# Kernel optimization log

Hardware: AMD Instinct MI355X
Metric: run time of the kernel (lower is better)

The kernel has to match this reference:

```python
import jax, jax.numpy as jnp
import numpy as np

# dims matching init_kwargs
U, T, S, K = 2048, 200, 10, 20   # users, history_length, slate_size, num_topics
DE, DU, V, H = 32, 32, 100000, 16  # doc_embed_dim, user_embed_dim, num_docs, rnn hidden
D_IN = DE + (S + 1) + (S + 1) * K + 1  # 264 concatenated feature width
LEAKY_ALPHA = 0.3  # keras LeakyReLU default


def setup_inputs() -> dict:
    key = jax.random.key(0)
    ks = jax.random.split(key, 9)
    slate_doc_quality_history = jax.random.normal(ks[0], (U, T, S), jnp.float32)
    slate_doc_features_history = jax.random.normal(ks[1], (U, T, S, K), jnp.float32)
    docid_history = jax.random.randint(ks[2], (U, T), 0, V + 1)  # 0 is the masked id
    ctime_history = jax.random.uniform(ks[3], (U, T), jnp.float32)
    # learned parameters
    emb_table = jax.random.normal(ks[4], (V + 1, DE), jnp.float32) * 0.05
    Wx = jax.random.normal(ks[5], (D_IN, H), jnp.float32) * (1.0 / np.sqrt(D_IN))
    Wh = jax.random.normal(ks[6], (H, H), jnp.float32) * (1.0 / np.sqrt(H))
    b_rnn = jnp.zeros((H,), jnp.float32)
    Wd = jax.random.normal(ks[7], (H, DU), jnp.float32) * (1.0 / np.sqrt(H))
    b_dense = jnp.zeros((DU,), jnp.float32)
    return dict(
        slate_doc_quality_history=slate_doc_quality_history,
        slate_doc_features_history=slate_doc_features_history,
        docid_history=docid_history,
        ctime_history=ctime_history,
        emb_table=emb_table, Wx=Wx, Wh=Wh, b_rnn=b_rnn, Wd=Wd, b_dense=b_dense,
    )


def reference(slate_doc_quality_history, slate_doc_features_history, docid_history,
              ctime_history, emb_table, Wx, Wh, b_rnn, Wd, b_dense):
    B, Tlen = docid_history.shape
    # embedding lookup; mask_zero=True -> timesteps with id==0 are skipped by the RNN
    emb = emb_table[docid_history]                                   # [U,T,DE]
    mask = docid_history != 0                                        # [U,T]
    # append zero quality column -> [U,T,S+1]
    q = jnp.concatenate([slate_doc_quality_history,
                         jnp.zeros((B, Tlen, 1), slate_doc_quality_history.dtype)], axis=-1)
    # append zero feature row on slate axis, flatten -> [U,T,(S+1)*K]
    f = jnp.concatenate([slate_doc_features_history,
                         jnp.zeros((B, Tlen, 1, K), slate_doc_features_history.dtype)], axis=-2)
    f = f.reshape(B, Tlen, -1)
    x = jnp.concatenate([emb, q, f, ctime_history[..., None]], axis=-1)  # [U,T,D_IN]

    # SimpleRNN(16): h_t = tanh(x_t Wx + h_{t-1} Wh + b); masked steps keep previous h
    pre = jnp.einsum('btd,dh->bth', x, Wx) + b_rnn                   # [U,T,H]

    def step(h, inp):
        pre_t, m_t = inp                                             # [U,H], [U]
        h_new = jnp.tanh(pre_t + h @ Wh)
        h = jnp.where(m_t[:, None], h_new, h)
        return h, None

    h0 = jnp.zeros((B, Wh.shape[0]), x.dtype)
    hT, _ = jax.lax.scan(step, h0, (pre.transpose(1, 0, 2), mask.T))
    # LeakyReLU(alpha=0.3) then Dense -> user embeddings [U, DU]
    a = jnp.where(hT >= 0, hT, LEAKY_ALPHA * hT)
    return a @ Wd + b_dense
```

## Files before the change

kernel.cpp:

```cpp
#include <hip/hip_runtime.h>

#define U_   2048
#define T_   200
#define H_   16
#define DU_  32
#define KP   288

typedef __attribute__((ext_vector_type(8))) short bf16x8;
typedef __attribute__((ext_vector_type(4))) float f32x4;

__device__ __forceinline__ unsigned short bf16_rne(float x) {
    unsigned u = __float_as_uint(x);
    return (unsigned short)((u + 0x7FFFu + ((u >> 16) & 1u)) >> 16);
}

__device__ __forceinline__ void cvt8(const float* x, bf16x8& hi, bf16x8& lo) {
    union { bf16x8 v; unsigned u[4]; } H, L;
#pragma unroll
    for (int i = 0; i < 4; ++i) {
        const unsigned short h0 = bf16_rne(x[2 * i]), h1 = bf16_rne(x[2 * i + 1]);
        const float r0 = x[2 * i]     - __uint_as_float((unsigned)h0 << 16);
        const float r1 = x[2 * i + 1] - __uint_as_float((unsigned)h1 << 16);
        H.u[i] = (unsigned)h0 | ((unsigned)h1 << 16);
        L.u[i] = (unsigned)bf16_rne(r0) | ((unsigned)bf16_rne(r1) << 16);
    }
    hi = H.v; lo = L.v;
}

__global__ __launch_bounds__(256) void k_wprep(
    const float* __restrict__ Wx,
    unsigned short* __restrict__ WThi, unsigned short* __restrict__ WTlo)
{
    const int idx = blockIdx.x * 256 + threadIdx.x;
    if (idx >= 16 * KP) return;
    const int n = idx / KP, k = idx - n * KP;
    const int s = k >> 5, kk = k & 31;
    float wv = 0.f;
    if (s < 7)       { if (k < 200) wv = Wx[(43 + k) * H_ + n]; }
    else if (s == 7) { wv = Wx[kk * H_ + n]; }
    else             { if (kk < 10) wv = Wx[(32 + kk) * H_ + n];
                       else if (kk == 10) wv = Wx[263 * H_ + n]; }
    const unsigned short h = bf16_rne(wv);
    WThi[idx] = h;
    WTlo[idx] = bf16_rne(wv - __uint_as_float((unsigned)h << 16));
}

__global__ __launch_bounds__(256, 3) void k_pre(
    const float* __restrict__ qh, const float* __restrict__ f,
    const int* __restrict__ docid, const float* __restrict__ ct,
    const float* __restrict__ emb,
    const unsigned short* __restrict__ WThi,
    const unsigned short* __restrict__ WTlo,
    const float* __restrict__ brnn, float* __restrict__ pre)
{
    __shared__ float pane[4][16 * 204];
    const int t = threadIdx.x, l = t & 63, w = t >> 6;
    const int tile = blockIdx.x * 4 + w;
    const int rbase = tile * 16;
    const int r = l & 15, qd = l >> 4;
    const int pos = rbase + r;

    const char* fsrc = (const char*)f + (size_t)rbase * 800;
    float4 buf[13];
#pragma unroll
    for (int m = 0; m < 13; ++m)
        if (m < 12 || l < 32)
            buf[m] = *(const float4*)(fsrc + (size_t)(m * 64 + l) * 16);

    const int did = docid[pos];
    const float4 e0 = *(const float4*)(emb + (size_t)did * 32 + qd * 8);
    const float4 e1 = *(const float4*)(emb + (size_t)did * 32 + qd * 8 + 4);

    float qx[8];
#pragma unroll
    for (int i = 0; i < 8; ++i) qx[i] = 0.f;
    if (qd == 0) {
#pragma unroll
        for (int j = 0; j < 4; ++j) {
            float2 v = *(const float2*)(qh + (size_t)pos * 10 + 2 * j);
            qx[2 * j] = v.x; qx[2 * j + 1] = v.y;
        }
    } else if (qd == 1) {
        qx[0] = qh[(size_t)pos * 10 + 8];
        qx[1] = qh[(size_t)pos * 10 + 9];
        qx[2] = ct[pos];
    }
    const float bias = brnn[r];

    float* pn = pane[w];
#pragma unroll
    for (int m = 0; m < 13; ++m) {
        const int g = m * 64 + l;
        if (g < 800) *(float4*)(pn + 4 * (g + g / 50)) = buf[m];
    }

    f32x4 acc = {bias, bias, bias, bias};

#pragma unroll
    for (int s = 0; s < 7; ++s) {
        float xr[8];
        if (s < 6 || qd == 0) {
            const float4 a0 = *(const float4*)(pn + r * 204 + s * 32 + qd * 8);
            const float4 a1 = *(const float4*)(pn + r * 204 + s * 32 + qd * 8 + 4);
            xr[0] = a0.x; xr[1] = a0.y; xr[2] = a0.z; xr[3] = a0.w;
            xr[4] = a1.x; xr[5] = a1.y; xr[6] = a1.z; xr[7] = a1.w;
        } else {
#pragma unroll
            for (int i = 0; i < 8; ++i) xr[i] = 0.f;
        }
        bf16x8 ah, al; cvt8(xr, ah, al);
        const bf16x8 bh = *(const bf16x8*)(WThi + r * KP + s * 32 + qd * 8);
        const bf16x8 bl = *(const bf16x8*)(WTlo + r * KP + s * 32 + qd * 8);
        acc = __builtin_amdgcn_mfma_f32_16x16x32_bf16(ah, bh, acc, 0, 0, 0);
        acc = __builtin_amdgcn_mfma_f32_16x16x32_bf16(al, bh, acc, 0, 0, 0);
        acc = __builtin_amdgcn_mfma_f32_16x16x32_bf16(ah, bl, acc, 0, 0, 0);
    }

    {
        float xr[8] = {e0.x, e0.y, e0.z, e0.w, e1.x, e1.y, e1.z, e1.w};
        bf16x8 ah, al; cvt8(xr, ah, al);
        const bf16x8 bh = *(const bf16x8*)(WThi + r * KP + 7 * 32 + qd * 8);
        const bf16x8 bl = *(const bf16x8*)(WTlo + r * KP + 7 * 32 + qd * 8);
        acc = __builtin_amdgcn_mfma_f32_16x16x32_bf16(ah, bh, acc, 0, 0, 0);
        acc = __builtin_amdgcn_mfma_f32_16x16x32_bf16(al, bh, acc, 0, 0, 0);
        acc = __builtin_amdgcn_mfma_f32_16x16x32_bf16(ah, bl, acc, 0, 0, 0);
    }
    {
        bf16x8 ah, al; cvt8(qx, ah, al);
        const bf16x8 bh = *(const bf16x8*)(WThi + r * KP + 8 * 32 + qd * 8);
        const bf16x8 bl = *(const bf16x8*)(WTlo + r * KP + 8 * 32 + qd * 8);
        acc = __builtin_amdgcn_mfma_f32_16x16x32_bf16(ah, bh, acc, 0, 0, 0);
        acc = __builtin_amdgcn_mfma_f32_16x16x32_bf16(al, bh, acc, 0, 0, 0);
        acc = __builtin_amdgcn_mfma_f32_16x16x32_bf16(ah, bl, acc, 0, 0, 0);
    }

#pragma unroll
    for (int i = 0; i < 4; ++i)
        pre[(size_t)(rbase + qd * 4 + i) * H_ + r] = acc[i];
}

__device__ __forceinline__ float tanh_fast(float x) {
    float e = __expf(2.f * x);
    return 1.f - 2.f / (e + 1.f);
}

__global__ __launch_bounds__(64) void k_rnn(
    const float* __restrict__ pre, const int* __restrict__ docid,
    const float* __restrict__ Wh, const float* __restrict__ Wd,
    const float* __restrict__ bd, float* __restrict__ out)
{
    const int tid = threadIdx.x;
    const int l = tid & 15;
    const int u = (blockIdx.x * 64 + tid) >> 4;

    const float* prow = pre + (size_t)u * T_ * H_;
    const int* drow = docid + (size_t)u * T_;

    float wh[16];
#pragma unroll
    for (int k = 0; k < 16; ++k) wh[k] = Wh[((l ^ k) << 4) | l];

    float h = 0.f;

    float pb0 = prow[0 * H_ + l], pb1 = prow[1 * H_ + l],
          pb2 = prow[2 * H_ + l], pb3 = prow[3 * H_ + l];
    int   m0 = drow[0], m1 = drow[1], m2 = drow[2], m3 = drow[3];

    for (int tb = 0; tb < T_; tb += 4) {
#pragma unroll
        for (int s = 0; s < 4; ++s) {
            float p; int m;
            if      (s == 0) { p = pb0; m = m0; }
            else if (s == 1) { p = pb1; m = m1; }
            else if (s == 2) { p = pb2; m = m2; }
            else             { p = pb3; m = m3; }

            int tn = tb + 4 + s; if (tn > T_ - 1) tn = T_ - 1;
            float pn = prow[tn * H_ + l];
            int   mn = drow[tn];
            if      (s == 0) { pb0 = pn; m0 = mn; }
            else if (s == 1) { pb1 = pn; m1 = mn; }
            else if (s == 2) { pb2 = pn; m2 = mn; }
            else             { pb3 = pn; m3 = mn; }

            float a0 = p, a1 = 0.f, a2 = 0.f, a3 = 0.f;
#pragma unroll
            for (int k = 0; k < 16; k += 4) {
                a0 += __shfl_xor(h, k + 0, 16) * wh[k + 0];
                a1 += __shfl_xor(h, k + 1, 16) * wh[k + 1];
                a2 += __shfl_xor(h, k + 2, 16) * wh[k + 2];
                a3 += __shfl_xor(h, k + 3, 16) * wh[k + 3];
            }
            float accv = (a0 + a1) + (a2 + a3);
            float th = tanh_fast(accv);
            h = (m != 0) ? th : h;
        }
    }

    float a = (h >= 0.f) ? h : 0.3f * h;

    float wd0[16], wd1[16];
#pragma unroll
    for (int k = 0; k < 16; ++k) {
        int j = l ^ k;
        wd0[k] = Wd[j * DU_ + l];
        wd1[k] = Wd[j * DU_ + l + 16];
    }
    float o0 = bd[l], o1 = bd[l + 16];
#pragma unroll
    for (int k = 0; k < 16; ++k) {
        float av = __shfl_xor(a, k, 16);
        o0 += av * wd0[k];
        o1 += av * wd1[k];
    }
    out[(size_t)u * DU_ + l] = o0;
    out[(size_t)u * DU_ + l + 16] = o1;
}

extern "C" void kernel_launch(void* const* d_in, const int* in_sizes, int n_in,
                              void* d_out, int out_size, void* d_ws, size_t ws_size,
                              hipStream_t stream) {
    const float* qh    = (const float*)d_in[0];
    const float* f     = (const float*)d_in[1];
    const int*   docid = (const int*)  d_in[2];
    const float* ct    = (const float*)d_in[3];
    const float* emb   = (const float*)d_in[4];
    const float* Wx    = (const float*)d_in[5];
    const float* Wh    = (const float*)d_in[6];
    const float* brnn  = (const float*)d_in[7];
    const float* Wd    = (const float*)d_in[8];
    const float* bd    = (const float*)d_in[9];
    float* out = (float*)d_out;

    float* pre = (float*)d_ws;
    unsigned short* WThi = (unsigned short*)((char*)d_ws + (size_t)U_ * T_ * H_ * 4);
    unsigned short* WTlo = WThi + 16 * KP;

    k_wprep<<<(16 * KP + 255) / 256, 256, 0, stream>>>(Wx, WThi, WTlo);
    k_pre<<<(U_ * T_) / 64, 256, 0, stream>>>(qh, f, docid, ct, emb, WThi, WTlo, brnn, pre);
    k_rnn<<<(U_ * H_) / 64, 64, 0, stream>>>(pre, docid, Wh, Wd, bd, out);
}
```

Before: 153.2 us.

## Make k_pre waves loop over multiple tiles with register prefetch of next tile

Each wave in the input-projection kernel now processes 8 consecutive 16-row tiles instead of one. Inside the loop it issues the global loads for the next tile's features, quality, ctime and embedding rows before running the MFMA work on the current tile, so load latency overlaps compute. The grid shrinks by the same factor of 8. The trade-off is fewer resident waves to hide memory latency, plus more live registers for the double-buffered data.

```diff
diff --git a/kernel.cpp b/kernel.cpp
--- a/kernel.cpp
+++ b/kernel.cpp
@@ -5,6 +5,7 @@
 #define H_   16
 #define DU_  32
 #define KP   288
+#define NT   8
 
 typedef __attribute__((ext_vector_type(8))) short bf16x8;
 typedef __attribute__((ext_vector_type(4))) float f32x4;
@@ -55,88 +56,118 @@
 {
     __shared__ float pane[4][16 * 204];
     const int t = threadIdx.x, l = t & 63, w = t >> 6;
-    const int tile = blockIdx.x * 4 + w;
-    const int rbase = tile * 16;
+    const int wid = blockIdx.x * 4 + w;
+    const int tbase = wid * NT;
     const int r = l & 15, qd = l >> 4;
-    const int pos = rbase + r;
-
-    const char* fsrc = (const char*)f + (size_t)rbase * 800;
+
+    float* pn = pane[w];
+    const char* fB = (const char*)f;
+    const float bias = brnn[r];
+
     float4 buf[13];
-#pragma unroll
-    for (int m = 0; m < 13; ++m)
-        if (m < 12 || l < 32)
-            buf[m] = *(const float4*)(fsrc + (size_t)(m * 64 + l) * 16);
-
-    const int did = docid[pos];
-    const float4 e0 = *(const float4*)(emb + (size_t)did * 32 + qd * 8);
-    const float4 e1 = *(const float4*)(emb + (size_t)did * 32 + qd * 8 + 4);
-
+    float4 e0, e1;
     float qx[8];
-#pragma unroll
-    for (int i = 0; i < 8; ++i) qx[i] = 0.f;
-    if (qd == 0) {
-#pragma unroll
-        for (int j = 0; j < 4; ++j) {
-            float2 v = *(const float2*)(qh + (size_t)pos * 10 + 2 * j);
-            qx[2 * j] = v.x; qx[2 * j + 1] = v.y;
-        }
-    } else if (qd == 1) {
-        qx[0] = qh[(size_t)pos * 10 + 8];
-        qx[1] = qh[(size_t)pos * 10 + 9];
-        qx[2] = ct[pos];
-    }
-    const float bias = brnn[r];
-
-    float* pn = pane[w];
-#pragma unroll
-    for (int m = 0; m < 13; ++m) {
-        const int g = m * 64 + l;
-        if (g < 800) *(float4*)(pn + 4 * (g + g / 50)) = buf[m];
-    }
-
-    f32x4 acc = {bias, bias, bias, bias};
-
-#pragma unroll
-    for (int s = 0; s < 7; ++s) {
-        float xr[8];
-        if (s < 6 || qd == 0) {
-            const float4 a0 = *(const float4*)(pn + r * 204 + s * 32 + qd * 8);
-            const float4 a1 = *(const float4*)(pn + r * 204 + s * 32 + qd * 8 + 4);
-            xr[0] = a0.x; xr[1] = a0.y; xr[2] = a0.z; xr[3] = a0.w;
-            xr[4] = a1.x; xr[5] = a1.y; xr[6] = a1.z; xr[7] = a1.w;
-        } else {
-#pragma unroll
-            for (int i = 0; i < 8; ++i) xr[i] = 0.f;
-        }
-        bf16x8 ah, al; cvt8(xr, ah, al);
-        const bf16x8 bh = *(const bf16x8*)(WThi + r * KP + s * 32 + qd * 8);
-        const bf16x8 bl = *(const bf16x8*)(WTlo + r * KP + s * 32 + qd * 8);
-        acc = __builtin_amdgcn_mfma_f32_16x16x32_bf16(ah, bh, acc, 0, 0, 0);
-        acc = __builtin_amdgcn_mfma_f32_16x16x32_bf16(al, bh, acc, 0, 0, 0);
-        acc = __builtin_amdgcn_mfma_f32_16x16x32_bf16(ah, bl, acc, 0, 0, 0);
-    }
+    int did_nxt = 0;
+
+    auto LOADF = [&](int tile) {
+#pragma unroll
+        for (int m = 0; m < 13; ++m)
+            if (m < 12 || l < 32)
+                buf[m] = *(const float4*)(fB + (size_t)tile * 12800 + (size_t)(m * 64 + l) * 16);
+    };
+    auto LOADQ = [&](int tile, float* dst) {
+        const int pos = tile * 16 + r;
+#pragma unroll
+        for (int j = 0; j < 8; ++j) dst[j] = 0.f;
+        if (qd == 0) {
+#pragma unroll
+            for (int j = 0; j < 4; ++j) {
+                float2 v = *(const float2*)(qh + (size_t)pos * 10 + 2 * j);
+                dst[2 * j] = v.x; dst[2 * j + 1] = v.y;
+            }
+        } else if (qd == 1) {
+            dst[0] = qh[(size_t)pos * 10 + 8];
+            dst[1] = qh[(size_t)pos * 10 + 9];
+            dst[2] = ct[pos];
+        }
+    };
 
     {
-        float xr[8] = {e0.x, e0.y, e0.z, e0.w, e1.x, e1.y, e1.z, e1.w};
-        bf16x8 ah, al; cvt8(xr, ah, al);
-        const bf16x8 bh = *(const bf16x8*)(WThi + r * KP + 7 * 32 + qd * 8);
-        const bf16x8 bl = *(const bf16x8*)(WTlo + r * KP + 7 * 32 + qd * 8);
-        acc = __builtin_amdgcn_mfma_f32_16x16x32_bf16(ah, bh, acc, 0, 0, 0);
-        acc = __builtin_amdgcn_mfma_f32_16x16x32_bf16(al, bh, acc, 0, 0, 0);
-        acc = __builtin_amdgcn_mfma_f32_16x16x32_bf16(ah, bl, acc, 0, 0, 0);
-    }
-    {
-        bf16x8 ah, al; cvt8(qx, ah, al);
-        const bf16x8 bh = *(const bf16x8*)(WThi + r * KP + 8 * 32 + qd * 8);
-        const bf16x8 bl = *(const bf16x8*)(WTlo + r * KP + 8 * 32 + qd * 8);
-        acc = __builtin_amdgcn_mfma_f32_16x16x32_bf16(ah, bh, acc, 0, 0, 0);
-        acc = __builtin_amdgcn_mfma_f32_16x16x32_bf16(al, bh, acc, 0, 0, 0);
-        acc = __builtin_amdgcn_mfma_f32_16x16x32_bf16(ah, bl, acc, 0, 0, 0);
-    }
-
-#pragma unroll
-    for (int i = 0; i < 4; ++i)
-        pre[(size_t)(rbase + qd * 4 + i) * H_ + r] = acc[i];
+        const int did0 = docid[tbase * 16 + r];
+        LOADF(tbase);
+        LOADQ(tbase, qx);
+        e0 = *(const float4*)(emb + (size_t)did0 * 32 + qd * 8);
+        e1 = *(const float4*)(emb + (size_t)did0 * 32 + qd * 8 + 4);
+        if (NT > 1) did_nxt = docid[(tbase + 1) * 16 + r];
+    }
+
+#pragma unroll 1
+    for (int i = 0; i < NT; ++i) {
+        const int rbase = (tbase + i) * 16;
+
+#pragma unroll
+        for (int m = 0; m < 13; ++m) {
+            const int g = m * 64 + l;
+            if (g < 800) *(float4*)(pn + 4 * (g + g / 50)) = buf[m];
+        }
+
+        const float4 ce0 = e0, ce1 = e1;
+        float cq[8];
+#pragma unroll
+        for (int j = 0; j < 8; ++j) cq[j] = qx[j];
+
+        if (i + 1 < NT) {
+            LOADF(tbase + i + 1);
+            LOADQ(tbase + i + 1, qx);
+            const int dd = did_nxt;
+            e0 = *(const float4*)(emb + (size_t)dd * 32 + qd * 8);
+            e1 = *(const float4*)(emb + (size_t)dd * 32 + qd * 8 + 4);
+            if (i + 2 < NT) did_nxt = docid[(tbase + i + 2) * 16 + r];
+        }
+
+        f32x4 acc = {bias, bias, bias, bias};
+
+#pragma unroll
+        for (int s = 0; s < 7; ++s) {
+            float xr[8];
+            if (s < 6 || qd == 0) {
+                const float4 a0 = *(const float4*)(pn + r * 204 + s * 32 + qd * 8);
+                const float4 a1 = *(const float4*)(pn + r * 204 + s * 32 + qd * 8 + 4);
+                xr[0] = a0.x; xr[1] = a0.y; xr[2] = a0.z; xr[3] = a0.w;
+                xr[4] = a1.x; xr[5] = a1.y; xr[6] = a1.z; xr[7] = a1.w;
+            } else {
+#pragma unroll
+                for (int j = 0; j < 8; ++j) xr[j] = 0.f;
+            }
+            bf16x8 ah, al; cvt8(xr, ah, al);
+            const bf16x8 bh = *(const bf16x8*)(WThi + r * KP + s * 32 + qd * 8);
+            const bf16x8 bl = *(const bf16x8*)(WTlo + r * KP + s * 32 + qd * 8);
+            acc = __builtin_amdgcn_mfma_f32_16x16x32_bf16(ah, bh, acc, 0, 0, 0);
+            acc = __builtin_amdgcn_mfma_f32_16x16x32_bf16(al, bh, acc, 0, 0, 0);
+            acc = __builtin_amdgcn_mfma_f32_16x16x32_bf16(ah, bl, acc, 0, 0, 0);
+        }
+        {
+            float xr[8] = {ce0.x, ce0.y, ce0.z, ce0.w, ce1.x, ce1.y, ce1.z, ce1.w};
+            bf16x8 ah, al; cvt8(xr, ah, al);
+            const bf16x8 bh = *(const bf16x8*)(WThi + r * KP + 7 * 32 + qd * 8);
+            const bf16x8 bl = *(const bf16x8*)(WTlo + r * KP + 7 * 32 + qd * 8);
+            acc = __builtin_amdgcn_mfma_f32_16x16x32_bf16(ah, bh, acc, 0, 0, 0);
+            acc = __builtin_amdgcn_mfma_f32_16x16x32_bf16(al, bh, acc, 0, 0, 0);
+            acc = __builtin_amdgcn_mfma_f32_16x16x32_bf16(ah, bl, acc, 0, 0, 0);
+        }
+        {
+            bf16x8 ah, al; cvt8(cq, ah, al);
+            const bf16x8 bh = *(const bf16x8*)(WThi + r * KP + 8 * 32 + qd * 8);
+            const bf16x8 bl = *(const bf16x8*)(WTlo + r * KP + 8 * 32 + qd * 8);
+            acc = __builtin_amdgcn_mfma_f32_16x16x32_bf16(ah, bh, acc, 0, 0, 0);
+            acc = __builtin_amdgcn_mfma_f32_16x16x32_bf16(al, bh, acc, 0, 0, 0);
+            acc = __builtin_amdgcn_mfma_f32_16x16x32_bf16(ah, bl, acc, 0, 0, 0);
+        }
+
+#pragma unroll
+        for (int ii = 0; ii < 4; ++ii)
+            pre[(size_t)(rbase + qd * 4 + ii) * H_ + r] = acc[ii];
+    }
 }
 
 __device__ __forceinline__ float tanh_fast(float x) {
@@ -237,6 +268,6 @@
     unsigned short* WTlo = WThi + 16 * KP;
 
     k_wprep<<<(16 * KP + 255) / 256, 256, 0, stream>>>(Wx, WThi, WTlo);
-    k_pre<<<(U_ * T_) / 64, 256, 0, stream>>>(qh, f, docid, ct, emb, WThi, WTlo, brnn, pre);
+    k_pre<<<(U_ * T_) / (64 * NT), 256, 0, stream>>>(qh, f, docid, ct, emb, WThi, WTlo, brnn, pre);
     k_rnn<<<(U_ * H_) / 64, 64, 0, stream>>>(pre, docid, Wh, Wd, bd, out);
 }
```

Result: slower. 356.9 us (+133.0%).

## Double-buffer feature tiles via direct global-to-LDS loads in persistent k_pre waves

Applied to the files above, without the earlier changes.

Restructures k_pre so each single-wave block processes eight 16-row tiles in a loop. The next tile's features are prefetched straight into LDS with global_load_lds while the current tile goes through the MFMAs. An XOR swizzle on the LDS layout replaces the old padded layout to avoid bank conflicts. The aim is to hide the latency of the dominant feature stream and drop the register round-trip; the cost is fewer, smaller blocks and a full vmcnt(0) wait every iteration.

```diff
diff --git a/kernel.cpp b/kernel.cpp
--- a/kernel.cpp
+++ b/kernel.cpp
@@ -5,6 +5,7 @@
 #define H_   16
 #define DU_  32
 #define KP   288
+#define NT   8
 
 typedef __attribute__((ext_vector_type(8))) short bf16x8;
 typedef __attribute__((ext_vector_type(4))) float f32x4;
@@ -25,6 +26,12 @@
         L.u[i] = (unsigned)bf16_rne(r0) | ((unsigned)bf16_rne(r1) << 16);
     }
     hi = H.v; lo = L.v;
+}
+
+__device__ __forceinline__ void g2l16(const void* g, void* l) {
+    __builtin_amdgcn_global_load_lds(
+        (const __attribute__((address_space(1))) void*)g,
+        (__attribute__((address_space(3))) void*)l, 16, 0, 0);
 }
 
 __global__ __launch_bounds__(256) void k_wprep(
@@ -45,7 +52,7 @@
     WTlo[idx] = bf16_rne(wv - __uint_as_float((unsigned)h << 16));
 }
 
-__global__ __launch_bounds__(256, 3) void k_pre(
+__global__ __launch_bounds__(64) void k_pre(
     const float* __restrict__ qh, const float* __restrict__ f,
     const int* __restrict__ docid, const float* __restrict__ ct,
     const float* __restrict__ emb,
@@ -53,90 +60,117 @@
     const unsigned short* __restrict__ WTlo,
     const float* __restrict__ brnn, float* __restrict__ pre)
 {
-    __shared__ float pane[4][16 * 204];
-    const int t = threadIdx.x, l = t & 63, w = t >> 6;
-    const int tile = blockIdx.x * 4 + w;
-    const int rbase = tile * 16;
+    __shared__ float pane[2][13 * 64 * 4];
+    const int l = threadIdx.x;
     const int r = l & 15, qd = l >> 4;
-    const int pos = rbase + r;
-
-    const char* fsrc = (const char*)f + (size_t)rbase * 800;
-    float4 buf[13];
-#pragma unroll
-    for (int m = 0; m < 13; ++m)
-        if (m < 12 || l < 32)
-            buf[m] = *(const float4*)(fsrc + (size_t)(m * 64 + l) * 16);
-
-    const int did = docid[pos];
-    const float4 e0 = *(const float4*)(emb + (size_t)did * 32 + qd * 8);
-    const float4 e1 = *(const float4*)(emb + (size_t)did * 32 + qd * 8 + 4);
-
-    float qx[8];
-#pragma unroll
-    for (int i = 0; i < 8; ++i) qx[i] = 0.f;
-    if (qd == 0) {
-#pragma unroll
-        for (int j = 0; j < 4; ++j) {
-            float2 v = *(const float2*)(qh + (size_t)pos * 10 + 2 * j);
-            qx[2 * j] = v.x; qx[2 * j + 1] = v.y;
-        }
-    } else if (qd == 1) {
-        qx[0] = qh[(size_t)pos * 10 + 8];
-        qx[1] = qh[(size_t)pos * 10 + 9];
-        qx[2] = ct[pos];
-    }
+    const int tbase = blockIdx.x * NT;
+    const char* fB = (const char*)f;
+
+    int off[13];
+#pragma unroll
+    for (int m = 0; m < 13; ++m) {
+        const int slot = m * 64 + l;
+        if (slot < 800) {
+            const int p = slot / 50, g2 = slot - 50 * p;
+            const int gr = (g2 < 48) ? (g2 ^ (p & 7)) : g2;
+            off[m] = p * 800 + gr * 16;
+        } else off[m] = 0;
+    }
+
+    auto STAGE = [&](int tile, int b) {
+        const char* src = fB + (size_t)tile * 12800;
+        char* dst = (char*)pane[b];
+#pragma unroll
+        for (int m = 0; m < 13; ++m)
+            g2l16(src + off[m], dst + m * 1024);
+    };
+
     const float bias = brnn[r];
-
-    float* pn = pane[w];
-#pragma unroll
-    for (int m = 0; m < 13; ++m) {
-        const int g = m * 64 + l;
-        if (g < 800) *(float4*)(pn + 4 * (g + g / 50)) = buf[m];
-    }
-
-    f32x4 acc = {bias, bias, bias, bias};
-
-#pragma unroll
-    for (int s = 0; s < 7; ++s) {
-        float xr[8];
-        if (s < 6 || qd == 0) {
-            const float4 a0 = *(const float4*)(pn + r * 204 + s * 32 + qd * 8);
-            const float4 a1 = *(const float4*)(pn + r * 204 + s * 32 + qd * 8 + 4);
-            xr[0] = a0.x; xr[1] = a0.y; xr[2] = a0.z; xr[3] = a0.w;
-            xr[4] = a1.x; xr[5] = a1.y; xr[6] = a1.z; xr[7] = a1.w;
-        } else {
-#pragma unroll
-            for (int i = 0; i < 8; ++i) xr[i] = 0.f;
-        }
-        bf16x8 ah, al; cvt8(xr, ah, al);
-        const bf16x8 bh = *(const bf16x8*)(WThi + r * KP + s * 32 + qd * 8);
-        const bf16x8 bl = *(const bf16x8*)(WTlo + r * KP + s * 32 + qd * 8);
-        acc = __builtin_amdgcn_mfma_f32_16x16x32_bf16(ah, bh, acc, 0, 0, 0);
-        acc = __builtin_amdgcn_mfma_f32_16x16x32_bf16(al, bh, acc, 0, 0, 0);
-        acc = __builtin_amdgcn_mfma_f32_16x16x32_bf16(ah, bl, acc, 0, 0, 0);
-    }
-
-    {
-        float xr[8] = {e0.x, e0.y, e0.z, e0.w, e1.x, e1.y, e1.z, e1.w};
-        bf16x8 ah, al; cvt8(xr, ah, al);
-        const bf16x8 bh = *(const bf16x8*)(WThi + r * KP + 7 * 32 + qd * 8);
-        const bf16x8 bl = *(const bf16x8*)(WTlo + r * KP + 7 * 32 + qd * 8);
-        acc = __builtin_amdgcn_mfma_f32_16x16x32_bf16(ah, bh, acc, 0, 0, 0);
-        acc = __builtin_amdgcn_mfma_f32_16x16x32_bf16(al, bh, acc, 0, 0, 0);
-        acc = __builtin_amdgcn_mfma_f32_16x16x32_bf16(ah, bl, acc, 0, 0, 0);
-    }
-    {
-        bf16x8 ah, al; cvt8(qx, ah, al);
-        const bf16x8 bh = *(const bf16x8*)(WThi + r * KP + 8 * 32 + qd * 8);
-        const bf16x8 bl = *(const bf16x8*)(WTlo + r * KP + 8 * 32 + qd * 8);
-        acc = __builtin_amdgcn_mfma_f32_16x16x32_bf16(ah, bh, acc, 0, 0, 0);
-        acc = __builtin_amdgcn_mfma_f32_16x16x32_bf16(al, bh, acc, 0, 0, 0);
-        acc = __builtin_amdgcn_mfma_f32_16x16x32_bf16(ah, bl, acc, 0, 0, 0);
-    }
-
-#pragma unroll
-    for (int i = 0; i < 4; ++i)
-        pre[(size_t)(rbase + qd * 4 + i) * H_ + r] = acc[i];
+    int did = docid[tbase * 16 + r];
+
+    STAGE(tbase, 0);
+
+#pragma unroll 1
+    for (int i = 0; i < NT; ++i) {
+        const int cur = i & 1;
+        asm volatile("s_waitcnt vmcnt(0)" ::: "memory");
+        __builtin_amdgcn_sched_barrier(0);
+
+        if (i + 1 < NT) STAGE(tbase + i + 1, cur ^ 1);
+
+        const int pos = (tbase + i) * 16 + r;
+        const float4 e0 = *(const float4*)(emb + (size_t)did * 32 + qd * 8);
+        const float4 e1 = *(const float4*)(emb + (size_t)did * 32 + qd * 8 + 4);
+        int did_n = did;
+        if (i + 1 < NT) did_n = docid[(tbase + i + 1) * 16 + r];
+        float qx[8];
+#pragma unroll
+        for (int j = 0; j < 8; ++j) qx[j] = 0.f;
+        if (qd == 0) {
+#pragma unroll
+            for (int j = 0; j < 4; ++j) {
+                float2 v = *(const float2*)(qh + (size_t)pos * 10 + 2 * j);
+                qx[2 * j] = v.x; qx[2 * j + 1] = v.y;
+            }
+        } else if (qd == 1) {
+            qx[0] = qh[(size_t)pos * 10 + 8];
+            qx[1] = qh[(size_t)pos * 10 + 9];
+            qx[2] = ct[pos];
+        }
+
+        const float4* pc = (const float4*)pane[cur];
+        f32x4 acc = {bias, bias, bias, bias};
+
+#pragma unroll
+        for (int s = 0; s < 7; ++s) {
+            float xr[8];
+            if (s < 6) {
+                const int a0 = 50 * r + ((8 * s + 2 * qd) ^ (r & 7));
+                const float4 v0 = pc[a0];
+                const float4 v1 = pc[a0 ^ 1];
+                xr[0] = v0.x; xr[1] = v0.y; xr[2] = v0.z; xr[3] = v0.w;
+                xr[4] = v1.x; xr[5] = v1.y; xr[6] = v1.z; xr[7] = v1.w;
+            } else if (qd == 0) {
+                const float4 v0 = pc[50 * r + 48];
+                const float4 v1 = pc[50 * r + 49];
+                xr[0] = v0.x; xr[1] = v0.y; xr[2] = v0.z; xr[3] = v0.w;
+                xr[4] = v1.x; xr[5] = v1.y; xr[6] = v1.z; xr[7] = v1.w;
+            } else {
+#pragma unroll
+                for (int j = 0; j < 8; ++j) xr[j] = 0.f;
+            }
+            bf16x8 ah, al; cvt8(xr, ah, al);
+            const bf16x8 bh = *(const bf16x8*)(WThi + r * KP + s * 32 + qd * 8);
+            const bf16x8 bl = *(const bf16x8*)(WTlo + r * KP + s * 32 + qd * 8);
+            acc = __builtin_amdgcn_mfma_f32_16x16x32_bf16(ah, bh, acc, 0, 0, 0);
+            acc = __builtin_amdgcn_mfma_f32_16x16x32_bf16(al, bh, acc, 0, 0, 0);
+            acc = __builtin_amdgcn_mfma_f32_16x16x32_bf16(ah, bl, acc, 0, 0, 0);
+        }
+        {
+            float xr[8] = {e0.x, e0.y, e0.z, e0.w, e1.x, e1.y, e1.z, e1.w};
+            bf16x8 ah, al; cvt8(xr, ah, al);
+            const bf16x8 bh = *(const bf16x8*)(WThi + r * KP + 7 * 32 + qd * 8);
+            const bf16x8 bl = *(const bf16x8*)(WTlo + r * KP + 7 * 32 + qd * 8);
+            acc = __builtin_amdgcn_mfma_f32_16x16x32_bf16(ah, bh, acc, 0, 0, 0);
+            acc = __builtin_amdgcn_mfma_f32_16x16x32_bf16(al, bh, acc, 0, 0, 0);
+            acc = __builtin_amdgcn_mfma_f32_16x16x32_bf16(ah, bl, acc, 0, 0, 0);
+        }
+        {
+            bf16x8 ah, al; cvt8(qx, ah, al);
+            const bf16x8 bh = *(const bf16x8*)(WThi + r * KP + 8 * 32 + qd * 8);
+            const bf16x8 bl = *(const bf16x8*)(WTlo + r * KP + 8 * 32 + qd * 8);
+            acc = __builtin_amdgcn_mfma_f32_16x16x32_bf16(ah, bh, acc, 0, 0, 0);
+            acc = __builtin_amdgcn_mfma_f32_16x16x32_bf16(al, bh, acc, 0, 0, 0);
+            acc = __builtin_amdgcn_mfma_f32_16x16x32_bf16(ah, bl, acc, 0, 0, 0);
+        }
+
+        const int rbase = (tbase + i) * 16;
+#pragma unroll
+        for (int ii = 0; ii < 4; ++ii)
+            pre[(size_t)(rbase + qd * 4 + ii) * H_ + r] = acc[ii];
+
+        did = did_n;
+    }
 }
 
 __device__ __forceinline__ float tanh_fast(float x) {
@@ -237,6 +271,6 @@
     unsigned short* WTlo = WThi + 16 * KP;
 
     k_wprep<<<(16 * KP + 255) / 256, 256, 0, stream>>>(Wx, WThi, WTlo);
-    k_pre<<<(U_ * T_) / 64, 256, 0, stream>>>(qh, f, docid, ct, emb, WThi, WTlo, brnn, pre);
+    k_pre<<<(U_ * T_) / (16 * NT), 64, 0, stream>>>(qh, f, docid, ct, emb, WThi, WTlo, brnn, pre);
     k_rnn<<<(U_ * H_) / 64, 64, 0, stream>>>(pre, docid, Wh, Wd, bd, out);
 }
```

Measured after the change: 182.0 us. 18.8% more time.
